# Optimization experiments

Measured on AMD Instinct MI355X. Metric: run time of the kernel, lower is better.

Reference implementation:

```python
import jax, jax.numpy as jnp
import numpy as np

N = 20000       # nodes
E = 100000      # edges
STEPS = 4
ND = 128        # node feature dim
ED = 128        # edge feature dim
NIN = 128       # node input dim
EIN = 291       # edge input dim (2 + 17*17)
H = 64          # mpn edge-mlp hidden


def _lin(x, w, b):
    return x @ w + b


def setup_inputs():
    key = jax.random.key(0)
    ks = jax.random.split(key, 16)

    def w(k, i, o):
        return (jax.random.normal(k, (i, o), jnp.float32) / np.float32(np.sqrt(i)))

    d = {}
    d["x"] = jax.random.normal(ks[0], (N, NIN), jnp.float32)
    d["edge_attr"] = jax.random.normal(ks[1], (E, EIN), jnp.float32)
    d["edge_index"] = jax.random.randint(ks[2], (2, E), 0, N, jnp.int32)
    # node embedding MLP: NIN -> 128 -> ND (ReLU between, none after last)
    d["new0"] = w(ks[3], NIN, 128); d["neb0"] = jnp.zeros(128, jnp.float32)
    d["new1"] = w(ks[4], 128, ND); d["neb1"] = jnp.zeros(ND, jnp.float32)
    # edge embedding MLP: EIN -> 64 -> ED
    d["eew0"] = w(ks[5], EIN, 64); d["eeb0"] = jnp.zeros(64, jnp.float32)
    d["eew1"] = w(ks[6], 64, ED); d["eeb1"] = jnp.zeros(ED, jnp.float32)
    # MPN edge MLP (skip=True): 2*(2*ND) + 2*ED = 768 -> 64 -> ED, ReLU after each
    d["mew0"] = w(ks[7], 4 * ND + 2 * ED, H); d["meb0"] = jnp.zeros(H, jnp.float32)
    d["mew1"] = w(ks[8], H, ED); d["meb1"] = jnp.zeros(ED, jnp.float32)
    # MPN node MLP: 2*ND + ED = 384 -> ND, ReLU
    d["mnw0"] = w(ks[9], 2 * ND + ED, ND); d["mnb0"] = jnp.zeros(ND, jnp.float32)
    # classification MLP: ED -> 64 -> 32 -> 1
    d["cw0"] = w(ks[10], ED, 64); d["cb0"] = jnp.zeros(64, jnp.float32)
    d["cw1"] = w(ks[11], 64, 32); d["cb1"] = jnp.zeros(32, jnp.float32)
    d["cw2"] = w(ks[12], 32, 1); d["cb2"] = jnp.zeros(1, jnp.float32)
    return d


def reference(x, edge_attr, edge_index,
              new0, neb0, new1, neb1,
              eew0, eeb0, eew1, eeb1,
              mew0, meb0, mew1, meb1,
              mnw0, mnb0,
              cw0, cb0, cw1, cb1, cw2, cb2):
    relu = jax.nn.relu
    j, i = edge_index[0], edge_index[1]  # j: source, i: target

    nf = _lin(relu(_lin(x, new0, neb0)), new1, neb1)          # [N, ND]
    ef = _lin(relu(_lin(edge_attr, eew0, eeb0)), eew1, eeb1)  # [E, ED]
    nf0, ef0 = nf, ef

    for _ in range(STEPS):
        # skip connections: concat initial features
        nfc = jnp.concatenate([nf0, nf], axis=1)  # [N, 2*ND]
        efc = jnp.concatenate([ef0, ef], axis=1)  # [E, 2*ED]
        x_i = nfc[i]  # [E, 2*ND] target
        x_j = nfc[j]  # [E, 2*ND] source
        # edge update MLP (ReLU after both layers)
        h = relu(_lin(jnp.concatenate([x_i, x_j, efc], axis=1), mew0, meb0))
        ef = relu(_lin(h, mew1, meb1))  # [E, ED]
        # message: mlp_node([x_i, edge_attr_new]) aggregated at target i
        msg = relu(_lin(jnp.concatenate([x_i, ef], axis=1), mnw0, mnb0))  # [E, ND]
        nf = jax.ops.segment_sum(msg, i, num_segments=N)  # [N, ND]

    out = relu(_lin(ef, cw0, cb0))
    out = relu(_lin(out, cw1, cb1))
    out = _lin(out, cw2, cb2)  # [E, 1]
    return out
```

## Files before the change

kernel.cpp:

```cpp
#include <hip/hip_runtime.h>
#include <hip/hip_bf16.h>

#define ND 128
#define ED 128
#define NIN 128
#define EIN 291
#define KPAD 320
#define HH 64
#define TM 32
#define TS 64
#define GSE 768
#define MAXGE 3

typedef __attribute__((ext_vector_type(8))) short short8;
typedef __attribute__((ext_vector_type(4))) float float4_;

__device__ __forceinline__ unsigned short f2bf(float f)
{
    union { float f; unsigned u; } v; v.f = f;
    unsigned u = v.u;
    unsigned r = (u + 0x7FFFu + ((u >> 16) & 1u)) >> 16;
    return (unsigned short)r;
}
__device__ __forceinline__ float bf2f(unsigned short s)
{
    union { unsigned u; float f; } v; v.u = ((unsigned)s) << 16;
    return v.f;
}

template<int T, int KC, int K>
__device__ __forceinline__ void stage_frags(const unsigned short* __restrict__ src,
                                            unsigned short* __restrict__ wreg,
                                            int t, int k0)
{
    constexpr int TOT = T * KC * 64;
#pragma unroll
    for (int it = 0; it < TOT / 256; it++) {
        int idx = it * 256 + t;
        int f = idx >> 6, l = idx & 63;
        int col = (f / KC) * 16 + (l & 15);
        int k = (f % KC) * 32 + ((l >> 4) * 8);
        *(short8*)&wreg[idx * 8] = *(const short8*)&src[(size_t)col * K + k0 + k];
    }
}
#define FRAG(wreg, f, lane) (*(const short8*)&(wreg)[(((f) << 6) + (lane)) * 8])

__global__ __launch_bounds__(256) void zero_k(float* __restrict__ p, int n4)
{
    int idx = blockIdx.x * 256 + threadIdx.x;
    if (idx < n4) ((float4*)p)[idx] = make_float4(0.f, 0.f, 0.f, 0.f);
}

__global__ __launch_bounds__(256) void hist_k(const int* __restrict__ tgti,
                                              int* __restrict__ deg, int E)
{
    int e = blockIdx.x * 256 + threadIdx.x;
    if (e < E) atomicAdd(&deg[tgti[e]], 1);
}

__global__ __launch_bounds__(256) void scan_k(const int* __restrict__ deg,
                                              int* __restrict__ row_ptr,
                                              int* __restrict__ cursor, int N, int E)
{
    __shared__ int part[256];
    const int t = threadIdx.x;
    const int chunk = (N + 255) / 256;
    const int base = t * chunk;
    int s = 0;
    for (int k = 0; k < chunk; k++) { int idx = base + k; if (idx < N) s += deg[idx]; }
    part[t] = s;
    __syncthreads();
    for (int off = 1; off < 256; off <<= 1) {
        int v = (t >= off) ? part[t - off] : 0;
        __syncthreads();
        part[t] += v;
        __syncthreads();
    }
    int run = (t == 0) ? 0 : part[t - 1];
    for (int k = 0; k < chunk; k++) {
        int idx = base + k;
        if (idx < N) { row_ptr[idx] = run; cursor[idx] = run; run += deg[idx]; }
    }
    if (t == 255) row_ptr[N] = E;
}

__global__ __launch_bounds__(256) void scatter_k(const int* __restrict__ tgti,
                                                 int* __restrict__ cursor,
                                                 int* __restrict__ csr_eid, int E)
{
    int e = blockIdx.x * 256 + threadIdx.x;
    if (e < E) {
        int p = atomicAdd(&cursor[tgti[e]], 1);
        csr_eid[p] = e;
    }
}

__global__ __launch_bounds__(256) void permidx_k(const int* __restrict__ csr_eid,
                                                 const int* __restrict__ srcj,
                                                 const int* __restrict__ tgti,
                                                 int* __restrict__ srcp,
                                                 int* __restrict__ tgtp, int E)
{
    int p = blockIdx.x * 256 + threadIdx.x;
    if (p < E) {
        int e = csr_eid[p];
        srcp[p] = srcj[e];
        tgtp[p] = tgti[e];
    }
}

__global__ __launch_bounds__(256) void agg_k(const int* __restrict__ row_ptr,
                                             const unsigned short* __restrict__ msg,
                                             unsigned short* __restrict__ nf_bf, int N)
{
    int n = blockIdx.x * 2 + (threadIdx.x >> 7);
    int c = threadIdx.x & 127;
    if (n >= N) return;
    int beg = row_ptr[n], end = row_ptr[n + 1];
    float acc = 0.f;
    for (int p = beg; p < end; p++)
        acc += bf2f(msg[(size_t)p * ND + c]);
    nf_bf[(size_t)n * ND + c] = f2bf(acc);
}

__global__ __launch_bounds__(256) void wprep_k(
    const float* __restrict__ mew0, const float* __restrict__ mew1, const float* __restrict__ mnw0,
    const float* __restrict__ eew0, const float* __restrict__ eew1, const float* __restrict__ cw0,
    const float* __restrict__ new0, const float* __restrict__ new1,
    unsigned short* __restrict__ w0T, unsigned short* __restrict__ w1T,
    unsigned short* __restrict__ wmT, unsigned short* __restrict__ w0eT,
    unsigned short* __restrict__ w1eT, unsigned short* __restrict__ cw0T,
    unsigned short* __restrict__ w0nT, unsigned short* __restrict__ w1nT)
{
    int idx = blockIdx.x * 256 + threadIdx.x;
    if (idx < 49152) {
        int c = idx / 768, k = idx % 768;
        w0T[idx] = f2bf(mew0[k * 64 + c]);
    } else if (idx < 57344) {
        int j = idx - 49152; int c = j / 64, k = j % 64;
        w1T[j] = f2bf(mew1[k * 128 + c]);
    } else if (idx < 106496) {
        int j = idx - 57344; int c = j / 384, k = j % 384;
        wmT[j] = f2bf(mnw0[k * 128 + c]);
    } else if (idx < 126976) {
        int j = idx - 106496; int c = j / KPAD, k = j % KPAD;
        w0eT[j] = (k < EIN) ? f2bf(eew0[k * 64 + c]) : (unsigned short)0;
    } else if (idx < 135168) {
        int j = idx - 126976; int c = j / 64, k = j % 64;
        w1eT[j] = f2bf(eew1[k * 128 + c]);
    } else if (idx < 143360) {
        int j = idx - 135168; int c = j / 128, k = j % 128;
        cw0T[j] = f2bf(cw0[k * 64 + c]);
    } else if (idx < 159744) {
        int j = idx - 143360; int c = j / 128, k = j % 128;
        w0nT[j] = f2bf(new0[k * 128 + c]);
    } else if (idx < 176128) {
        int j = idx - 159744; int c = j / 128, k = j % 128;
        w1nT[j] = f2bf(new1[k * 128 + c]);
    }
}

__global__ __launch_bounds__(256) void node_embed_k(
    const float* __restrict__ x,
    const unsigned short* __restrict__ w0nT, const float* __restrict__ b0,
    const unsigned short* __restrict__ w1nT, const float* __restrict__ b1,
    unsigned short* __restrict__ nf0_bf, unsigned short* __restrict__ nf_bf, int N)
{
    const int t = threadIdx.x;
    const int n0 = blockIdx.x * TM;
    __shared__ unsigned short wreg[8192];
    __shared__ unsigned short xin[TM][130];
    __shared__ unsigned short h_bf[TM][130];

#pragma unroll
    for (int it = 0; it < 4; it++) {
        int idx = it * 256 + t;
        int r = idx >> 5, c4 = idx & 31;
        int node = n0 + r; if (node >= N) node = N - 1;
        float4 v = *(const float4*)(x + (size_t)node * NIN + c4 * 4);
        unsigned lo = (unsigned)f2bf(v.x) | ((unsigned)f2bf(v.y) << 16);
        unsigned hi = (unsigned)f2bf(v.z) | ((unsigned)f2bf(v.w) << 16);
        *(uint2*)&xin[r][c4 * 4] = make_uint2(lo, hi);
    }

    const int w = t >> 6, lane = t & 63, quad = lane >> 4, n16 = lane & 15;
    const int m = w & 1, nh = w >> 1;

    float4_ acc[4];
#pragma unroll
    for (int q = 0; q < 4; q++) acc[q] = (float4_){0.f, 0.f, 0.f, 0.f};
#pragma unroll
    for (int hf = 0; hf < 2; hf++) {
        stage_frags<8, 2, 128>(w0nT, wreg, t, hf * 64);
        __syncthreads();
#pragma unroll
        for (int kc = 0; kc < 2; kc++) {
            short8 a = *(const short8*)&xin[m * 16 + n16][hf * 64 + kc * 32 + quad * 8];
#pragma unroll
            for (int tt = 0; tt < 4; tt++) {
                short8 b = FRAG(wreg, (nh * 4 + tt) * 2 + kc, lane);
                acc[tt] = __builtin_amdgcn_mfma_f32_16x16x32_bf16(a, b, acc[tt], 0, 0, 0);
            }
        }
        __syncthreads();
    }
#pragma unroll
    for (int tt = 0; tt < 4; tt++) {
        int c = nh * 64 + tt * 16 + n16;
        float bias = b0[c];
#pragma unroll
        for (int r4 = 0; r4 < 4; r4++)
            h_bf[m * 16 + quad * 4 + r4][c] = f2bf(fmaxf(acc[tt][r4] + bias, 0.f));
    }
    __syncthreads();

    float4_ acc2[4];
#pragma unroll
    for (int q = 0; q < 4; q++) acc2[q] = (float4_){0.f, 0.f, 0.f, 0.f};
#pragma unroll
    for (int hf = 0; hf < 2; hf++) {
        stage_frags<8, 2, 128>(w1nT, wreg, t, hf * 64);
        __syncthreads();
#pragma unroll
        for (int kc = 0; kc < 2; kc++) {
            short8 a = *(const short8*)&h_bf[m * 16 + n16][hf * 64 + kc * 32 + quad * 8];
#pragma unroll
            for (int tt = 0; tt < 4; tt++) {
                short8 b = FRAG(wreg, (nh * 4 + tt) * 2 + kc, lane);
                acc2[tt] = __builtin_amdgcn_mfma_f32_16x16x32_bf16(a, b, acc2[tt], 0, 0, 0);
            }
        }
        __syncthreads();
    }
#pragma unroll
    for (int tt = 0; tt < 4; tt++) {
        int c = nh * 64 + tt * 16 + n16;
        float bias = b1[c];
#pragma unroll
        for (int r4 = 0; r4 < 4; r4++) {
            int row = m * 16 + quad * 4 + r4;
            int node = n0 + row;
            if (node < N) {
                unsigned short v = f2bf(acc2[tt][r4] + bias);
                nf0_bf[(size_t)node * ND + c] = v;
                nf_bf[(size_t)node * ND + c] = v;
            }
        }
    }
}

__global__ __launch_bounds__(256, 3) void edge_embed_k(
    const float* __restrict__ ea, const int* __restrict__ csr_eid,
    const unsigned short* __restrict__ w0eT, const float* __restrict__ b0,
    const unsigned short* __restrict__ w1eT, const float* __restrict__ b1,
    unsigned short* __restrict__ ef0_bf, unsigned short* __restrict__ ef_bf,
    int E, int ntiles)
{
    const int t = threadIdx.x;
    __shared__ unsigned short w0reg[10240];
    __shared__ unsigned short w1reg[8192];
    __shared__ unsigned short hsl[4][16 * 66];

    const int w = t >> 6, lane = t & 63, quad = lane >> 4, n16 = lane & 15;

    stage_frags<8, 2, 64>(w1eT, w1reg, t, 0);

    int ng = 0;
    int tile[MAXGE];
#pragma unroll
    for (int g = 0; g < MAXGE; g++) {
        int tl = blockIdx.x + g * GSE;
        if (tl < ntiles) { tile[g] = tl; ng = g + 1; }
        else tile[g] = 0;
    }

    float4_ accL[MAXGE][4];
#pragma unroll
    for (int g = 0; g < MAXGE; g++)
#pragma unroll
        for (int q = 0; q < 4; q++) accL[g][q] = (float4_){0.f, 0.f, 0.f, 0.f};

#pragma unroll
    for (int hf = 0; hf < 2; hf++) {
        __syncthreads();
        stage_frags<4, 5, KPAD>(w0eT, w0reg, t, hf * 160);
        __syncthreads();
#pragma unroll
        for (int g = 0; g < MAXGE; g++) {
            if (g < ng) {
                int p = tile[g] * 64 + w * 16 + n16; if (p >= E) p = E - 1;
                const float* src = ea + (size_t)csr_eid[p] * EIN;
#pragma unroll
                for (int kc = 0; kc < 5; kc++) {
                    int k = hf * 160 + kc * 32 + quad * 8;
                    union { short8 s; uint4 u; } av;
                    if (k + 8 <= EIN) {
                        float4 v0 = *(const float4*)(src + k);
                        float4 v1 = *(const float4*)(src + k + 4);
                        av.u.x = (unsigned)f2bf(v0.x) | ((unsigned)f2bf(v0.y) << 16);
                        av.u.y = (unsigned)f2bf(v0.z) | ((unsigned)f2bf(v0.w) << 16);
                        av.u.z = (unsigned)f2bf(v1.x) | ((unsigned)f2bf(v1.y) << 16);
                        av.u.w = (unsigned)f2bf(v1.z) | ((unsigned)f2bf(v1.w) << 16);
                    } else {
                        unsigned short vv[8];
#pragma unroll
                        for (int j = 0; j < 8; j++)
                            vv[j] = (k + j < EIN) ? f2bf(src[k + j]) : (unsigned short)0;
                        av.u.x = (unsigned)vv[0] | ((unsigned)vv[1] << 16);
                        av.u.y = (unsigned)vv[2] | ((unsigned)vv[3] << 16);
                        av.u.z = (unsigned)vv[4] | ((unsigned)vv[5] << 16);
                        av.u.w = (unsigned)vv[6] | ((unsigned)vv[7] << 16);
                    }
#pragma unroll
                    for (int tt = 0; tt < 4; tt++) {
                        short8 b = FRAG(w0reg, tt * 5 + kc, lane);
                        accL[g][tt] = __builtin_amdgcn_mfma_f32_16x16x32_bf16(av.s, b, accL[g][tt], 0, 0, 0);
                    }
                }
            }
        }
    }

#pragma unroll
    for (int g = 0; g < MAXGE; g++) {
        if (g < ng) {
#pragma unroll
            for (int tt = 0; tt < 4; tt++) {
                int c = tt * 16 + n16;
                float bias = b0[c];
#pragma unroll
                for (int r4 = 0; r4 < 4; r4++)
                    hsl[w][(quad * 4 + r4) * 66 + c] = f2bf(fmaxf(accL[g][tt][r4] + bias, 0.f));
            }
            float4_ acc2[8];
#pragma unroll
            for (int q = 0; q < 8; q++) acc2[q] = (float4_){0.f, 0.f, 0.f, 0.f};
#pragma unroll
            for (int kc = 0; kc < 2; kc++) {
                short8 a2 = *(const short8*)&hsl[w][n16 * 66 + kc * 32 + quad * 8];
#pragma unroll
                for (int tt = 0; tt < 8; tt++)
                    acc2[tt] = __builtin_amdgcn_mfma_f32_16x16x32_bf16(
                        a2, FRAG(w1reg, tt * 2 + kc, lane), acc2[tt], 0, 0, 0);
            }
#pragma unroll
            for (int tt = 0; tt < 8; tt++) {
                int c = tt * 16 + n16;
                float bias = b1[c];
#pragma unroll
                for (int r4 = 0; r4 < 4; r4++) {
                    int p = tile[g] * 64 + w * 16 + quad * 4 + r4;
                    if (p < E) {
                        unsigned short v = f2bf(acc2[tt][r4] + bias);
                        ef0_bf[(size_t)p * ED + c] = v;
                        ef_bf[(size_t)p * ED + c] = v;
                    }
                }
            }
        }
    }
}

__global__ __launch_bounds__(256, 3) void edge_step_k(
    const int* __restrict__ srcp, const int* __restrict__ tgtp,
    const unsigned short* __restrict__ nf0_bf, const unsigned short* __restrict__ nf_bf,
    const unsigned short* __restrict__ ef0_bf, unsigned short* __restrict__ ef_bf,
    unsigned short* __restrict__ msg,
    const unsigned short* __restrict__ w0T, const float* __restrict__ meb0,
    const unsigned short* __restrict__ w1T, const float* __restrict__ meb1,
    const unsigned short* __restrict__ wmT, const float* __restrict__ mnb0,
    int E, int wmsg)
{
    const int t = threadIdx.x;
    const int e0 = blockIdx.x * TS;
    __shared__ unsigned short wreg[16384];
    __shared__ unsigned short hef[4][2080];

    const int w = t >> 6, lane = t & 63, quad = lane >> 4, n16 = lane & 15;
    int ec = e0 + w * 16 + n16; if (ec >= E) ec = E - 1;
    const int ti = tgtp[ec], sj = srcp[ec];

    const unsigned short* pA[6] = {
        nf0_bf + (size_t)ti * ND + quad * 8,
        nf_bf  + (size_t)ti * ND + quad * 8,
        nf0_bf + (size_t)sj * ND + quad * 8,
        nf_bf  + (size_t)sj * ND + quad * 8,
        ef0_bf + (size_t)ec * ED + quad * 8,
        ef_bf  + (size_t)ec * ED + quad * 8 };

    float4_ accL[4];
#pragma unroll
    for (int q = 0; q < 4; q++) accL[q] = (float4_){0.f, 0.f, 0.f, 0.f};
#pragma unroll
    for (int hf = 0; hf < 3; hf++) {
        short8 a8[8];
#pragma unroll
        for (int q2 = 0; q2 < 8; q2++)
            a8[q2] = *(const short8*)(pA[hf * 2 + (q2 >> 2)] + (q2 & 3) * 32);
        stage_frags<4, 8, 768>(w0T, wreg, t, hf * 256);
        __syncthreads();
#pragma unroll
        for (int kc = 0; kc < 8; kc++) {
#pragma unroll
            for (int tt = 0; tt < 4; tt++) {
                short8 b = FRAG(wreg, tt * 8 + kc, lane);
                accL[tt] = __builtin_amdgcn_mfma_f32_16x16x32_bf16(a8[kc], b, accL[tt], 0, 0, 0);
            }
        }
        __syncthreads();
    }

#pragma unroll
    for (int tt = 0; tt < 4; tt++) {
        int c = tt * 16 + n16;
        float bias = meb0[c];
#pragma unroll
        for (int r4 = 0; r4 < 4; r4++)
            hef[w][(quad * 4 + r4) * 66 + c] = f2bf(fmaxf(accL[tt][r4] + bias, 0.f));
    }

    stage_frags<8, 2, 64>(w1T, wreg, t, 0);
    __syncthreads();
    {
        float4_ acc[8];
#pragma unroll
        for (int q = 0; q < 8; q++) acc[q] = (float4_){0.f, 0.f, 0.f, 0.f};
#pragma unroll
        for (int kc = 0; kc < 2; kc++) {
            short8 a = *(const short8*)&hef[w][n16 * 66 + kc * 32 + quad * 8];
#pragma unroll
            for (int tt = 0; tt < 8; tt++) {
                short8 b = FRAG(wreg, tt * 2 + kc, lane);
                acc[tt] = __builtin_amdgcn_mfma_f32_16x16x32_bf16(a, b, acc[tt], 0, 0, 0);
            }
        }
#pragma unroll
        for (int tt = 0; tt < 8; tt++) {
            int c = tt * 16 + n16;
            float bias = meb1[c];
#pragma unroll
            for (int r4 = 0; r4 < 4; r4++) {
                int row = quad * 4 + r4;
                unsigned short v = f2bf(fmaxf(acc[tt][r4] + bias, 0.f));
                hef[w][row * 130 + c] = v;
                int e = e0 + w * 16 + row;
                if (e < E) ef_bf[(size_t)e * ED + c] = v;
            }
        }
    }
    __syncthreads();

    if (wmsg) {
        float4_ accM[8];
#pragma unroll
        for (int q = 0; q < 8; q++) accM[q] = (float4_){0.f, 0.f, 0.f, 0.f};
#pragma unroll
        for (int j = 0; j < 3; j++) {
            short8 a4[4];
            if (j < 2) {
#pragma unroll
                for (int q2 = 0; q2 < 4; q2++)
                    a4[q2] = *(const short8*)(pA[j] + q2 * 32);
            } else {
#pragma unroll
                for (int q2 = 0; q2 < 4; q2++)
                    a4[q2] = *(const short8*)&hef[w][n16 * 130 + q2 * 32 + quad * 8];
            }
            stage_frags<8, 4, 384>(wmT, wreg, t, j * 128);
            __syncthreads();
#pragma unroll
            for (int kc = 0; kc < 4; kc++) {
#pragma unroll
                for (int tt = 0; tt < 8; tt++) {
                    short8 b = FRAG(wreg, tt * 4 + kc, lane);
                    accM[tt] = __builtin_amdgcn_mfma_f32_16x16x32_bf16(a4[kc], b, accM[tt], 0, 0, 0);
                }
            }
            __syncthreads();
        }
#pragma unroll
        for (int tt = 0; tt < 8; tt++) {
            int c = tt * 16 + n16;
            float bias = mnb0[c];
#pragma unroll
            for (int r4 = 0; r4 < 4; r4++) {
                int row = w * 16 + quad * 4 + r4;
                int e = e0 + row;
                if (e < E)
                    msg[(size_t)e * ND + c] = f2bf(fmaxf(accM[tt][r4] + bias, 0.f));
            }
        }
    }
}

__global__ __launch_bounds__(256) void classify_k(
    const unsigned short* __restrict__ ef_bf, const int* __restrict__ csr_eid,
    const unsigned short* __restrict__ cw0T, const float* __restrict__ cb0,
    const float* __restrict__ cw1, const float* __restrict__ cb1,
    const float* __restrict__ cw2, const float* __restrict__ cb2,
    float* __restrict__ out, int E)
{
    const int t = threadIdx.x;
    const int e0 = blockIdx.x * TM;
    __shared__ unsigned short h0_bf[TM][66];
    __shared__ float h1[TM][33];

    const int w = t >> 6, lane = t & 63, quad = lane >> 4, n16 = lane & 15;
    const int m = w & 1;
    const int erow = m * 16 + n16;
    int ec = e0 + erow; if (ec >= E) ec = E - 1;
    const unsigned short* pa = ef_bf + (size_t)ec * ED + quad * 8;

    {
        const int cb = (w >> 1) * 32;
        float4_ acc0 = {0.f, 0.f, 0.f, 0.f}, acc1 = acc0;
        const unsigned short* b0p = cw0T + (size_t)(cb + n16) * 128 + quad * 8;
        const unsigned short* b1p = b0p + (size_t)16 * 128;
#pragma unroll
        for (int kc = 0; kc < 4; kc++) {
            short8 a  = *(const short8*)(pa + kc * 32);
            short8 bb0 = *(const short8*)(b0p + kc * 32);
            short8 bb1 = *(const short8*)(b1p + kc * 32);
            acc0 = __builtin_amdgcn_mfma_f32_16x16x32_bf16(a, bb0, acc0, 0, 0, 0);
            acc1 = __builtin_amdgcn_mfma_f32_16x16x32_bf16(a, bb1, acc1, 0, 0, 0);
        }
#pragma unroll
        for (int t2 = 0; t2 < 2; t2++) {
            int c = cb + t2 * 16 + n16;
            float bias = cb0[c];
            float4_ ac = t2 ? acc1 : acc0;
#pragma unroll
            for (int r4 = 0; r4 < 4; r4++)
                h0_bf[m * 16 + quad * 4 + r4][c] = f2bf(fmaxf(ac[r4] + bias, 0.f));
        }
    }
    __syncthreads();

    {
        int c = t & 31;
        int rbase = (t >> 5) * 4;
#pragma unroll
        for (int q = 0; q < 4; q++) {
            int r = rbase + q;
            float acc = cb1[c];
#pragma unroll 8
            for (int k = 0; k < 64; k++) acc += bf2f(h0_bf[r][k]) * cw1[k * 32 + c];
            h1[r][c] = fmaxf(acc, 0.f);
        }
    }
    __syncthreads();

    if (t < TM) {
        int p = e0 + t;
        if (p < E) {
            float a = cb2[0];
#pragma unroll
            for (int k = 0; k < 32; k++) a += h1[t][k] * cw2[k];
            out[csr_eid[p]] = a;
        }
    }
}

extern "C" void kernel_launch(void* const* d_in, const int* in_sizes, int n_in,
                              void* d_out, int out_size, void* d_ws, size_t ws_size,
                              hipStream_t stream)
{
    const float* x    = (const float*)d_in[0];
    const float* ea   = (const float*)d_in[1];
    const int*   eidx = (const int*)d_in[2];
    const float* new0 = (const float*)d_in[3];  const float* neb0 = (const float*)d_in[4];
    const float* new1 = (const float*)d_in[5];  const float* neb1 = (const float*)d_in[6];
    const float* eew0 = (const float*)d_in[7];  const float* eeb0 = (const float*)d_in[8];
    const float* eew1 = (const float*)d_in[9];  const float* eeb1 = (const float*)d_in[10];
    const float* mew0 = (const float*)d_in[11]; const float* meb0 = (const float*)d_in[12];
    const float* mew1 = (const float*)d_in[13]; const float* meb1 = (const float*)d_in[14];
    const float* mnw0 = (const float*)d_in[15]; const float* mnb0 = (const float*)d_in[16];
    const float* cw0  = (const float*)d_in[17]; const float* cb0  = (const float*)d_in[18];
    const float* cw1  = (const float*)d_in[19]; const float* cb1  = (const float*)d_in[20];
    const float* cw2  = (const float*)d_in[21]; const float* cb2  = (const float*)d_in[22];

    const int N = in_sizes[0] / NIN;
    const int E = in_sizes[2] / 2;
    const int* srcj = eidx;
    const int* tgti = eidx + E;

    char* wsb = (char*)d_ws;
    unsigned short* nf0_bf = (unsigned short*)wsb;
    unsigned short* nf_bf  = nf0_bf + (size_t)N * ND;
    unsigned short* ef0_bf = nf_bf + (size_t)N * ND;
    unsigned short* ef_bf  = ef0_bf + (size_t)E * ED;
    unsigned short* msg    = ef_bf + (size_t)E * ED;
    unsigned short* w0T  = msg + (size_t)E * ND;
    unsigned short* w1T  = w0T + 49152;
    unsigned short* wmT  = w1T + 8192;
    unsigned short* w0eT = wmT + 49152;
    unsigned short* w1eT = w0eT + 64 * KPAD;
    unsigned short* cw0T = w1eT + 8192;
    unsigned short* w0nT = cw0T + 8192;
    unsigned short* w1nT = w0nT + 16384;
    int* deg     = (int*)(w1nT + 16384);
    int* cursor  = deg + N;
    int* row_ptr = cursor + N;
    int* csr_eid = row_ptr + (N + 4);
    int* srcp    = csr_eid + E;
    int* tgtp    = srcp + E;

    const int eblocks32 = (E + TM - 1) / TM;
    const int nblocks32 = (N + TM - 1) / TM;
    const int ntiles64 = (E + 63) / 64;

    wprep_k<<<(176128 + 255) / 256, 256, 0, stream>>>(mew0, mew1, mnw0, eew0, eew1, cw0,
                                                      new0, new1,
                                                      w0T, w1T, wmT, w0eT, w1eT, cw0T,
                                                      w0nT, w1nT);

    zero_k<<<((2 * N) / 4 + 255) / 256, 256, 0, stream>>>((float*)deg, (2 * N) / 4);
    hist_k<<<(E + 255) / 256, 256, 0, stream>>>(tgti, deg, E);
    scan_k<<<1, 256, 0, stream>>>(deg, row_ptr, cursor, N, E);
    scatter_k<<<(E + 255) / 256, 256, 0, stream>>>(tgti, cursor, csr_eid, E);
    permidx_k<<<(E + 255) / 256, 256, 0, stream>>>(csr_eid, srcj, tgti, srcp, tgtp, E);

    node_embed_k<<<nblocks32, 256, 0, stream>>>(x, w0nT, neb0, w1nT, neb1,
                                                nf0_bf, nf_bf, N);
    edge_embed_k<<<GSE, 256, 0, stream>>>(ea, csr_eid, w0eT, eeb0, w1eT, eeb1,
                                          ef0_bf, ef_bf, E, ntiles64);

    for (int s = 0; s < 4; s++) {
        edge_step_k<<<ntiles64, 256, 0, stream>>>(srcp, tgtp, nf0_bf, nf_bf,
                                                  ef0_bf, ef_bf, msg,
                                                  w0T, meb0, w1T, meb1, wmT, mnb0,
                                                  E, (s < 3) ? 1 : 0);
        if (s < 3)
            agg_k<<<(N + 1) / 2, 256, 0, stream>>>(row_ptr, msg, nf_bf, N);
    }

    classify_k<<<eblocks32, 256, 0, stream>>>(ef_bf, csr_eid, cw0T, cb0, cw1, cb1, cw2, cb2,
                                              (float*)d_out, E);
}
```

Before: 729.5 us.

## Fuse segment-sum aggregation into edge step via in-tile segmented reduction

Instead of writing per-edge bf16 messages and running a separate CSR aggregation kernel, the edge step stages messages in shared memory and reduces them per target node within each 32-edge half tile. It writes node sums directly when a segment lies entirely in the half tile, and otherwise atomically adds into an fp32 buffer. A lightweight fixup kernel then converts those boundary segments to bf16 and clears the buffer. Node features are now ping-ponged between two buffers. This removes the E×128 message write and read, at the cost of atomics, extra shared-memory staging and a serial 32-row loop per thread.

```diff
diff --git a/kernel.cpp b/kernel.cpp
--- a/kernel.cpp
+++ b/kernel.cpp
@@ -109,18 +109,20 @@
     }
 }
 
-__global__ __launch_bounds__(256) void agg_k(const int* __restrict__ row_ptr,
-                                             const unsigned short* __restrict__ msg,
-                                             unsigned short* __restrict__ nf_bf, int N)
+__global__ __launch_bounds__(256) void fixup_k(const int* __restrict__ row_ptr,
+                                               float* __restrict__ nfx,
+                                               unsigned short* __restrict__ nf_out, int N)
 {
     int n = blockIdx.x * 2 + (threadIdx.x >> 7);
     int c = threadIdx.x & 127;
     if (n >= N) return;
     int beg = row_ptr[n], end = row_ptr[n + 1];
-    float acc = 0.f;
-    for (int p = beg; p < end; p++)
-        acc += bf2f(msg[(size_t)p * ND + c]);
-    nf_bf[(size_t)n * ND + c] = f2bf(acc);
+    if (beg == end) { nf_out[(size_t)n * ND + c] = 0; return; }
+    if ((beg >> 5) != ((end - 1) >> 5)) {
+        size_t idx = (size_t)n * ND + c;
+        nf_out[idx] = f2bf(nfx[idx]);
+        nfx[idx] = 0.f;
+    }
 }
 
 __global__ __launch_bounds__(256) void wprep_k(
@@ -363,9 +365,9 @@
 
 __global__ __launch_bounds__(256, 3) void edge_step_k(
     const int* __restrict__ srcp, const int* __restrict__ tgtp,
-    const unsigned short* __restrict__ nf0_bf, const unsigned short* __restrict__ nf_bf,
+    const unsigned short* __restrict__ nf0_bf, const unsigned short* __restrict__ nf_in,
     const unsigned short* __restrict__ ef0_bf, unsigned short* __restrict__ ef_bf,
-    unsigned short* __restrict__ msg,
+    unsigned short* __restrict__ nf_out, float* __restrict__ nfx,
     const unsigned short* __restrict__ w0T, const float* __restrict__ meb0,
     const unsigned short* __restrict__ w1T, const float* __restrict__ meb1,
     const unsigned short* __restrict__ wmT, const float* __restrict__ mnb0,
@@ -382,9 +384,9 @@
 
     const unsigned short* pA[6] = {
         nf0_bf + (size_t)ti * ND + quad * 8,
-        nf_bf  + (size_t)ti * ND + quad * 8,
+        nf_in  + (size_t)ti * ND + quad * 8,
         nf0_bf + (size_t)sj * ND + quad * 8,
-        nf_bf  + (size_t)sj * ND + quad * 8,
+        nf_in  + (size_t)sj * ND + quad * 8,
         ef0_bf + (size_t)ec * ED + quad * 8,
         ef_bf  + (size_t)ec * ED + quad * 8 };
 
@@ -478,6 +480,7 @@
             }
             __syncthreads();
         }
+
 #pragma unroll
         for (int tt = 0; tt < 8; tt++) {
             int c = tt * 16 + n16;
@@ -485,9 +488,34 @@
 #pragma unroll
             for (int r4 = 0; r4 < 4; r4++) {
                 int row = w * 16 + quad * 4 + r4;
-                int e = e0 + row;
-                if (e < E)
-                    msg[(size_t)e * ND + c] = f2bf(fmaxf(accM[tt][r4] + bias, 0.f));
+                wreg[row * 132 + c] = f2bf(fmaxf(accM[tt][r4] + bias, 0.f));
+            }
+        }
+        int* tg = (int*)&hef[0][0];
+        if (t < 66) {
+            int p = e0 - 1 + t;
+            tg[t] = (p >= 0 && p < E) ? tgtp[p] : -1;
+        }
+        __syncthreads();
+        {
+            int c = t & 127, half = t >> 7;
+            int r0 = half * 32;
+            float acc = 0.f;
+            int rs = 0;
+            for (int r = 0; r < 32; r++) {
+                int p = e0 + r0 + r;
+                if (p >= E) break;
+                int n = tg[r0 + r + 1];
+                acc += bf2f(wreg[(r0 + r) * 132 + c]);
+                bool end_here = (tg[r0 + r + 2] != n);
+                if (end_here) {
+                    bool beg_in = (rs > 0) || (tg[r0] != n);
+                    if (beg_in) nf_out[(size_t)n * ND + c] = f2bf(acc);
+                    else        atomicAdd(&nfx[(size_t)n * ND + c], acc);
+                    acc = 0.f; rs = r + 1;
+                } else if (r == 31) {
+                    atomicAdd(&nfx[(size_t)n * ND + c], acc);
+                }
             }
         }
     }
@@ -586,11 +614,13 @@
 
     char* wsb = (char*)d_ws;
     unsigned short* nf0_bf = (unsigned short*)wsb;
-    unsigned short* nf_bf  = nf0_bf + (size_t)N * ND;
-    unsigned short* ef0_bf = nf_bf + (size_t)N * ND;
+    unsigned short* nfA    = nf0_bf + (size_t)N * ND;
+    unsigned short* ef0_bf = nfA + (size_t)N * ND;
     unsigned short* ef_bf  = ef0_bf + (size_t)E * ED;
-    unsigned short* msg    = ef_bf + (size_t)E * ED;
-    unsigned short* w0T  = msg + (size_t)E * ND;
+    unsigned short* slot   = ef_bf + (size_t)E * ED;
+    unsigned short* nfB    = slot;
+    float*          nfx    = (float*)(slot + (size_t)N * ND);
+    unsigned short* w0T  = slot + (size_t)E * ND;
     unsigned short* w1T  = w0T + 49152;
     unsigned short* wmT  = w1T + 8192;
     unsigned short* w0eT = wmT + 49152;
@@ -620,18 +650,24 @@
     scatter_k<<<(E + 255) / 256, 256, 0, stream>>>(tgti, cursor, csr_eid, E);
     permidx_k<<<(E + 255) / 256, 256, 0, stream>>>(csr_eid, srcj, tgti, srcp, tgtp, E);
 
+    zero_k<<<((N * ND) / 4 + 255) / 256, 256, 0, stream>>>(nfx, (N * ND) / 4);
+
     node_embed_k<<<nblocks32, 256, 0, stream>>>(x, w0nT, neb0, w1nT, neb1,
-                                                nf0_bf, nf_bf, N);
+                                                nf0_bf, nfA, N);
     edge_embed_k<<<GSE, 256, 0, stream>>>(ea, csr_eid, w0eT, eeb0, w1eT, eeb1,
                                           ef0_bf, ef_bf, E, ntiles64);
 
+    unsigned short* nfR = nfA;
+    unsigned short* nfW = nfB;
     for (int s = 0; s < 4; s++) {
-        edge_step_k<<<ntiles64, 256, 0, stream>>>(srcp, tgtp, nf0_bf, nf_bf,
-                                                  ef0_bf, ef_bf, msg,
+        edge_step_k<<<ntiles64, 256, 0, stream>>>(srcp, tgtp, nf0_bf, nfR,
+                                                  ef0_bf, ef_bf, nfW, nfx,
                                                   w0T, meb0, w1T, meb1, wmT, mnb0,
                                                   E, (s < 3) ? 1 : 0);
-        if (s < 3)
-            agg_k<<<(N + 1) / 2, 256, 0, stream>>>(row_ptr, msg, nf_bf, N);
+        if (s < 3) {
+            fixup_k<<<(N + 1) / 2, 256, 0, stream>>>(row_ptr, nfx, nfW, N);
+            unsigned short* tmp = nfR; nfR = nfW; nfW = tmp;
+        }
     }
 
     classify_k<<<eblocks32, 256, 0, stream>>>(ef_bf, csr_eid, cw0T, cb0, cw1, cb1, cw2, cb2,
```

Result: faster. 680.2 us (-6.8%).
